# Kernel tuning notes

Measured on AMD Instinct MI355X. Metric: run time of the kernel, lower is better.

## Reference

```python
import jax, jax.numpy as jnp
import numpy as np

N_NODES = 50000
N_EDGES = 800000
N_GRAPHS = 128
IN_DIM = 256
OUT_DIM = 128
N_LAYERS = 3
NEG_SLOPE = 0.01  # nn.LeakyReLU default


def setup_inputs() -> dict:
    key = jax.random.key(0)
    ks = jax.random.split(key, 10)
    feat = jax.random.normal(ks[0], (N_NODES, IN_DIM), jnp.float32)
    src = jax.random.randint(ks[1], (N_EDGES,), 0, N_NODES, jnp.int32)
    dst = jax.random.randint(ks[2], (N_EDGES,), 0, N_NODES, jnp.int32)
    graph_ids = jnp.sort(jax.random.randint(ks[3], (N_NODES,), 0, N_GRAPHS, jnp.int32))
    s_in = 1.0 / np.sqrt(IN_DIM).astype(np.float32)
    s_out = 1.0 / np.sqrt(OUT_DIM).astype(np.float32)
    w_red = jax.random.uniform(ks[4], (IN_DIM, OUT_DIM), jnp.float32, -s_in, s_in)
    b_red = jax.random.uniform(ks[5], (OUT_DIM,), jnp.float32, -s_in, s_in)
    w_gcn = jax.random.uniform(ks[6], (N_LAYERS, OUT_DIM, OUT_DIM), jnp.float32, -s_out, s_out)
    b_gcn = jnp.zeros((N_LAYERS, OUT_DIM), jnp.float32)  # DGL GraphConv bias init = zeros
    w_cls = jax.random.uniform(ks[7], (OUT_DIM, 2), jnp.float32, -s_out, s_out)
    b_cls = jax.random.uniform(ks[8], (2,), jnp.float32, -s_out, s_out)
    return dict(feat=feat, src=src, dst=dst, graph_ids=graph_ids,
                w_red=w_red, b_red=b_red, w_gcn=w_gcn, b_gcn=b_gcn,
                w_cls=w_cls, b_cls=b_cls)


def _graph_conv(x, src, dst, w, b, out_norm, in_norm):
    # DGL GraphConv, norm='both': h = D_in^{-1/2} A D_out^{-1/2} x W + b
    xs = x * out_norm[:, None]                                   # [N, d] source normalization
    agg = jax.ops.segment_sum(xs[src], dst, num_segments=x.shape[0])  # gather -> scatter-add
    return (agg * in_norm[:, None]) @ w + b


def reference(feat, src, dst, graph_ids, w_red, b_red, w_gcn, b_gcn, w_cls, b_cls):
    n = feat.shape[0]
    ones = jnp.ones((src.shape[0],), feat.dtype)
    out_deg = jax.ops.segment_sum(ones, src, num_segments=n)
    in_deg = jax.ops.segment_sum(ones, dst, num_segments=n)
    out_norm = jnp.maximum(out_deg, 1.0) ** -0.5  # DGL clamps degree to >=1
    in_norm = jnp.maximum(in_deg, 1.0) ** -0.5
    h0 = feat @ w_red + b_red  # Dropout(0.2) in eval mode = identity
    # Faithful to source: every layer consumes h0 (node_features never updated);
    # only the last layer's activation survives the loop.
    out = h0
    for i in range(N_LAYERS):
        out = jax.nn.leaky_relu(
            _graph_conv(h0, src, dst, w_gcn[i], b_gcn[i], out_norm, in_norm), NEG_SLOPE)
    g = jax.ops.segment_sum(out, graph_ids, num_segments=N_GRAPHS)  # sum readout per graph
    return g @ w_cls + b_cls  # [N_GRAPHS, 2]
```

## Files before the change

kernel.cpp:

```cpp
#include <hip/hip_runtime.h>

#define N_NODES 50000
#define N_EDGES 800000
#define N_GRAPHS 128
#define IN_DIM 256
#define OUT_DIM 128
#define NEG_SLOPE 0.01f

#define RCHUNK 64
#define NB_SCAN ((N_NODES + 255) / 256)

#define NSLICE 4
#define SLICE 12544
#define NTOT (NSLICE * SLICE)
#define NCHUNK 64
#define NE4 (N_EDGES / 4)
#define QPC (NE4 / NCHUNK)

typedef __attribute__((ext_vector_type(8))) short bf16x8;
typedef __attribute__((ext_vector_type(4))) float f32x4;
typedef unsigned short ushort_t;
typedef unsigned int uint_t;

__device__ inline ushort_t f2b(float f) {
    union { float f; unsigned u; } c{f};
    unsigned r = c.u + 0x7FFFu + ((c.u >> 16) & 1u);
    return (ushort_t)(r >> 16);
}
__device__ inline float b2f(ushort_t u) {
    union { unsigned u; float f; } c{(unsigned)u << 16};
    return c.f;
}
__device__ inline float blo(uint_t v) {
    union { unsigned u; float f; } c{v << 16};
    return c.f;
}
__device__ inline float bhi(uint_t v) {
    union { unsigned u; float f; } c{v & 0xFFFF0000u};
    return c.f;
}

__global__ __launch_bounds__(256) void deg_kernel(const int4* __restrict__ src4,
                                                  const int4* __restrict__ dst4,
                                                  ushort_t* __restrict__ rep) {
    __shared__ int bins[SLICE];
    int b     = blockIdx.x;
    int hist  = b >> 8;
    int rem   = b & 255;
    int slice = rem >> 6;
    int chunk = rem & 63;
    const int4* ea = hist ? dst4 : src4;
    int lo = slice * SLICE;

    for (int i = threadIdx.x; i < SLICE; i += 256) bins[i] = 0;
    __syncthreads();

    int q0 = chunk * QPC;
    int q1 = q0 + QPC;
    for (int q = q0 + threadIdx.x; q < q1; q += 256) {
        int4 e = ea[q];
        unsigned a0 = (unsigned)(e.x - lo); if (a0 < SLICE) atomicAdd(&bins[a0], 1);
        unsigned a1 = (unsigned)(e.y - lo); if (a1 < SLICE) atomicAdd(&bins[a1], 1);
        unsigned a2 = (unsigned)(e.z - lo); if (a2 < SLICE) atomicAdd(&bins[a2], 1);
        unsigned a3 = (unsigned)(e.w - lo); if (a3 < SLICE) atomicAdd(&bins[a3], 1);
    }
    __syncthreads();

    uint_t* rp32 = (uint_t*)(rep + (size_t)(hist * NCHUNK + chunk) * NTOT + lo);
    for (int i = threadIdx.x; i < SLICE / 2; i += 256)
        rp32[i] = (uint_t)(bins[2 * i] | (bins[2 * i + 1] << 16));
}

__global__ __launch_bounds__(256) void norm_kernel(ushort_t* __restrict__ rep,
                                                   float* __restrict__ out_norm,
                                                   float* __restrict__ in_norm,
                                                   int* __restrict__ deg_in_tot,
                                                   int* __restrict__ bsum) {
    __shared__ int red[256];
    int t = threadIdx.x;
    int i = blockIdx.x * 256 + t;
    int si_keep = 0;
    if (i < N_NODES) {
        int so = 0;
#pragma unroll
        for (int c = 0; c < NCHUNK; ++c) so += rep[(size_t)c * NTOT + i];
        int si = 0;
#pragma unroll
        for (int c = 0; c < NCHUNK; ++c) {
            size_t off = (size_t)(NCHUNK + c) * NTOT + i;
            int v = rep[off];
            rep[off] = (ushort_t)si;
            si += v;
        }
        deg_in_tot[i] = si;
        si_keep = si;
        int dq = so > 1 ? so : 1;
        int di = si > 1 ? si : 1;
        out_norm[i] = rsqrtf((float)dq);
        in_norm[i]  = rsqrtf((float)di);
    }
    red[t] = si_keep;
    __syncthreads();
    for (int off = 128; off > 0; off >>= 1) {
        if (t < off) red[t] += red[t + off];
        __syncthreads();
    }
    if (t == 0) bsum[blockIdx.x] = red[0];
}

__global__ __launch_bounds__(256) void fill_kernel(const int* __restrict__ deg_in,
                                                   const int* __restrict__ bsum,
                                                   int* __restrict__ row_ofs) {
    __shared__ int sh[256];
    int t   = threadIdx.x;
    int bid = blockIdx.x;

    int v = (t < NB_SCAN) ? bsum[t] : 0;
    sh[t] = v;
    __syncthreads();
    for (int off = 1; off < 256; off <<= 1) {
        int a = sh[t];
        int b = (t >= off) ? sh[t - off] : 0;
        __syncthreads();
        sh[t] = a + b;
        __syncthreads();
    }
    int bofs  = sh[bid] - bsum[bid];
    int total = sh[NB_SCAN - 1];
    __syncthreads();

    int idx = bid * 256 + t;
    int dv  = (idx < N_NODES) ? deg_in[idx] : 0;
    sh[t] = dv;
    __syncthreads();
    for (int off = 1; off < 256; off <<= 1) {
        int a = sh[t];
        int b = (t >= off) ? sh[t - off] : 0;
        __syncthreads();
        sh[t] = a + b;
        __syncthreads();
    }
    if (idx < N_NODES) row_ofs[idx] = bofs + sh[t] - dv;
    if (bid == 0 && t == 0) row_ofs[N_NODES] = total;
}

__global__ __launch_bounds__(256) void build_kernel(const int4* __restrict__ src4,
                                                    const int4* __restrict__ dst4,
                                                    const int* __restrict__ row_ofs,
                                                    const ushort_t* __restrict__ rep,
                                                    int* __restrict__ esrc) {
    __shared__ int cur[SLICE];
    int b     = blockIdx.x;
    int slice = b >> 6;
    int chunk = b & 63;
    int lo    = slice * SLICE;
    const ushort_t* rel = rep + (size_t)(NCHUNK + chunk) * NTOT + lo;

    for (int i = threadIdx.x; i < SLICE; i += 256) {
        int n = lo + i;
        int r = (n < N_NODES) ? row_ofs[n] : 0;
        cur[i] = r + (int)rel[i];
    }
    __syncthreads();

    int q0 = chunk * QPC;
    int q1 = q0 + QPC;
    for (int q = q0 + threadIdx.x; q < q1; q += 256) {
        int4 s = src4[q];
        int4 d = dst4[q];
        unsigned a0 = (unsigned)(d.x - lo); if (a0 < SLICE) esrc[atomicAdd(&cur[a0], 1)] = s.x;
        unsigned a1 = (unsigned)(d.y - lo); if (a1 < SLICE) esrc[atomicAdd(&cur[a1], 1)] = s.y;
        unsigned a2 = (unsigned)(d.z - lo); if (a2 < SLICE) esrc[atomicAdd(&cur[a2], 1)] = s.z;
        unsigned a3 = (unsigned)(d.w - lo); if (a3 < SLICE) esrc[atomicAdd(&cur[a3], 1)] = s.w;
    }
}

__global__ __launch_bounds__(128) void wc_kernel(const float* __restrict__ w_red,
                                                 const float* __restrict__ b_red,
                                                 const float* __restrict__ w2,
                                                 ushort_t* __restrict__ Wcs,
                                                 float* __restrict__ bc,
                                                 float* __restrict__ g) {
    int j = threadIdx.x;
    int i = blockIdx.x;
    if (i < N_GRAPHS) g[i * OUT_DIM + j] = 0.f;
    const float* vin = (i < IN_DIM) ? (w_red + (size_t)i * OUT_DIM) : b_red;
    float s = 0.f;
    for (int k = 0; k < OUT_DIM; ++k) s = fmaf(vin[k], w2[k * OUT_DIM + j], s);
    if (i < IN_DIM) Wcs[(size_t)j * IN_DIM + i] = f2b(s);
    else            bc[j] = s;
}

__global__ __launch_bounds__(256) void gemm_z(const float* __restrict__ feat,
                                              const ushort_t* __restrict__ Wcs,
                                              const float* __restrict__ bc,
                                              const float* __restrict__ out_norm,
                                              ushort_t* __restrict__ zb) {
    __shared__ ushort_t Bs[64 * IN_DIM];
    int t    = threadIdx.x;
    int lane = t & 63;
    int wv   = t >> 6;
    int bm   = blockIdx.x * 64 + wv * 16;
    int bn0  = blockIdx.y * 64;
    int mrow = lane & 15;
    int kg   = lane >> 4;
    int gm   = bm + mrow;

    {
        const char* wsrc = (const char*)(Wcs + (size_t)bn0 * IN_DIM);
        char* bdst = (char*)Bs;
#pragma unroll
        for (int p = 0; p < 8; ++p) {
            int d  = p * 4096 + t * 16;
            int ds = d ^ (((d >> 9) & 7) << 4);
            *(int4*)(bdst + ds) = *(const int4*)(wsrc + d);
        }
    }
    __syncthreads();

    f32x4 acc[4];
#pragma unroll
    for (int nt = 0; nt < 4; ++nt) acc[nt] = (f32x4){0.f, 0.f, 0.f, 0.f};

    int boff[4];
#pragma unroll
    for (int nt = 0; nt < 4; ++nt) {
        int n = nt * 16 + mrow;
        boff[nt] = n * 512 + ((kg * 16) ^ ((n & 7) << 4));
    }
    const char* bsp = (const char*)Bs;

    bool valid = gm < N_NODES;
    const float* fp = feat + (size_t)(valid ? gm : 0) * IN_DIM + kg * 8;
    const float4 zf4 = make_float4(0.f, 0.f, 0.f, 0.f);

    float4 a0c = valid ? *(const float4*)(fp + 0) : zf4;
    float4 a1c = valid ? *(const float4*)(fp + 4) : zf4;
    float4 a0n = zf4, a1n = zf4;

#pragma unroll
    for (int kt = 0; kt < IN_DIM / 32; ++kt) {
        if (kt < IN_DIM / 32 - 1) {
            a0n = valid ? *(const float4*)(fp + (kt + 1) * 32) : zf4;
            a1n = valid ? *(const float4*)(fp + (kt + 1) * 32 + 4) : zf4;
        }
        bf16x8 af;
        af[0] = (short)f2b(a0c.x); af[1] = (short)f2b(a0c.y);
        af[2] = (short)f2b(a0c.z); af[3] = (short)f2b(a0c.w);
        af[4] = (short)f2b(a1c.x); af[5] = (short)f2b(a1c.y);
        af[6] = (short)f2b(a1c.z); af[7] = (short)f2b(a1c.w);
#pragma unroll
        for (int nt = 0; nt < 4; ++nt) {
            bf16x8 bf = *(const bf16x8*)(bsp + (boff[nt] ^ (kt << 6)));
            acc[nt] = __builtin_amdgcn_mfma_f32_16x16x32_bf16(af, bf, acc[nt], 0, 0, 0);
        }
        a0c = a0n; a1c = a1n;
    }

    float on[4];
#pragma unroll
    for (int r = 0; r < 4; ++r) {
        int row = bm + kg * 4 + r;
        on[r] = (row < N_NODES) ? out_norm[row] : 0.f;
    }
#pragma unroll
    for (int nt = 0; nt < 4; ++nt) {
        int col = bn0 + nt * 16 + mrow;
        float bcv = bc[col];
#pragma unroll
        for (int r = 0; r < 4; ++r) {
            int row = bm + kg * 4 + r;
            if (row < N_NODES)
                zb[(size_t)row * OUT_DIM + col] = f2b(on[r] * (acc[nt][r] + bcv));
        }
    }
}

__global__ __launch_bounds__(256) void gather_kernel(const uint4* __restrict__ zb4,
                                                     const int* __restrict__ esrc,
                                                     const int* __restrict__ row_ofs,
                                                     const float* __restrict__ in_norm,
                                                     const float* __restrict__ b2,
                                                     uint4* __restrict__ hb4) {
    int n      = blockIdx.x * 16 + (threadIdx.x >> 4);
    int lane16 = threadIdx.x & 15;
    int e0 = row_ofs[n];
    int e1 = row_ofs[n + 1];
    float ac[8];
#pragma unroll
    for (int i = 0; i < 8; ++i) ac[i] = 0.f;

    int e = e0;
    for (; e + 8 <= e1; e += 8) {
        uint4 v[8];
#pragma unroll
        for (int u = 0; u < 8; ++u) v[u] = zb4[(size_t)esrc[e + u] * 16 + lane16];
#pragma unroll
        for (int u = 0; u < 8; ++u) {
            ac[0] += blo(v[u].x); ac[1] += bhi(v[u].x);
            ac[2] += blo(v[u].y); ac[3] += bhi(v[u].y);
            ac[4] += blo(v[u].z); ac[5] += bhi(v[u].z);
            ac[6] += blo(v[u].w); ac[7] += bhi(v[u].w);
        }
    }
    if (e + 4 <= e1) {
        uint4 v[4];
#pragma unroll
        for (int u = 0; u < 4; ++u) v[u] = zb4[(size_t)esrc[e + u] * 16 + lane16];
#pragma unroll
        for (int u = 0; u < 4; ++u) {
            ac[0] += blo(v[u].x); ac[1] += bhi(v[u].x);
            ac[2] += blo(v[u].y); ac[3] += bhi(v[u].y);
            ac[4] += blo(v[u].z); ac[5] += bhi(v[u].z);
            ac[6] += blo(v[u].w); ac[7] += bhi(v[u].w);
        }
        e += 4;
    }
    for (; e < e1; ++e) {
        uint4 v = zb4[(size_t)esrc[e] * 16 + lane16];
        ac[0] += blo(v.x); ac[1] += bhi(v.x);
        ac[2] += blo(v.y); ac[3] += bhi(v.y);
        ac[4] += blo(v.z); ac[5] += bhi(v.z);
        ac[6] += blo(v.w); ac[7] += bhi(v.w);
    }

    float inn = in_norm[n];
    float4 bA = *(const float4*)&b2[lane16 * 8];
    float4 bB = *(const float4*)&b2[lane16 * 8 + 4];
    float hv[8];
    hv[0] = fmaf(inn, ac[0], bA.x); hv[1] = fmaf(inn, ac[1], bA.y);
    hv[2] = fmaf(inn, ac[2], bA.z); hv[3] = fmaf(inn, ac[3], bA.w);
    hv[4] = fmaf(inn, ac[4], bB.x); hv[5] = fmaf(inn, ac[5], bB.y);
    hv[6] = fmaf(inn, ac[6], bB.z); hv[7] = fmaf(inn, ac[7], bB.w);
#pragma unroll
    for (int i = 0; i < 8; ++i) hv[i] = (hv[i] > 0.f) ? hv[i] : NEG_SLOPE * hv[i];
    uint4 o;
    o.x = (uint_t)f2b(hv[0]) | ((uint_t)f2b(hv[1]) << 16);
    o.y = (uint_t)f2b(hv[2]) | ((uint_t)f2b(hv[3]) << 16);
    o.z = (uint_t)f2b(hv[4]) | ((uint_t)f2b(hv[5]) << 16);
    o.w = (uint_t)f2b(hv[6]) | ((uint_t)f2b(hv[7]) << 16);
    hb4[(size_t)n * 16 + lane16] = o;
}

__global__ __launch_bounds__(64) void readout_kernel(const uint_t* __restrict__ hb2,
                                                     const int* __restrict__ gids,
                                                     float* __restrict__ g) {
    int t    = threadIdx.x;
    int n0   = blockIdx.x * RCHUNK;
    int nend = n0 + RCHUNK;
    if (nend > N_NODES) nend = N_NODES;
    float acc0 = 0.f, acc1 = 0.f;
    int   cur = gids[n0];
    for (int n = n0; n < nend; ++n) {
        int gid = gids[n];
        if (gid != cur) {
            atomicAdd(&g[cur * OUT_DIM + 2 * t], acc0);
            atomicAdd(&g[cur * OUT_DIM + 2 * t + 1], acc1);
            acc0 = acc1 = 0.f;
            cur = gid;
        }
        uint_t v = hb2[(size_t)n * 64 + t];
        acc0 += blo(v);
        acc1 += bhi(v);
    }
    atomicAdd(&g[cur * OUT_DIM + 2 * t], acc0);
    atomicAdd(&g[cur * OUT_DIM + 2 * t + 1], acc1);
}

__global__ __launch_bounds__(256) void cls_kernel(const float* __restrict__ g,
                                                  const float* __restrict__ w_cls,
                                                  const float* __restrict__ b_cls,
                                                  float* __restrict__ out) {
    int t  = threadIdx.x;
    int gr = t >> 1;
    int c  = t & 1;
    float s = b_cls[c];
    for (int k = 0; k < OUT_DIM; ++k) s = fmaf(g[gr * OUT_DIM + k], w_cls[k * 2 + c], s);
    out[t] = s;
}

extern "C" void kernel_launch(void* const* d_in, const int* in_sizes, int n_in,
                              void* d_out, int out_size, void* d_ws, size_t ws_size,
                              hipStream_t stream) {
    const float* feat  = (const float*)d_in[0];
    const int*   src   = (const int*)d_in[1];
    const int*   dst   = (const int*)d_in[2];
    const int*   gids  = (const int*)d_in[3];
    const float* w_red = (const float*)d_in[4];
    const float* b_red = (const float*)d_in[5];
    const float* w_gcn = (const float*)d_in[6];
    const float* b_gcn = (const float*)d_in[7];
    const float* w_cls = (const float*)d_in[8];
    const float* b_cls = (const float*)d_in[9];
    float* out = (float*)d_out;

    float* z        = (float*)d_ws;
    float* h        = z + (size_t)N_NODES * OUT_DIM;
    float* out_norm = h + (size_t)N_NODES * OUT_DIM;
    float* in_norm  = out_norm + N_NODES;
    int*   deg_in   = (int*)(in_norm + N_NODES);
    int*   row_ofs  = deg_in + N_NODES;
    int*   esrc     = row_ofs + N_NODES + 1;
    int*   bsum     = esrc + N_EDGES;
    ushort_t* Wcs   = (ushort_t*)(bsum + NB_SCAN);
    float* bc       = (float*)(Wcs + IN_DIM * OUT_DIM);
    float* g        = bc + OUT_DIM;

    ushort_t* zb = (ushort_t*)z;
    ushort_t* hb = (ushort_t*)h;

    ushort_t* rep = (ushort_t*)z;

    const float* w2 = w_gcn + 2 * OUT_DIM * OUT_DIM;
    const float* b2 = b_gcn + 2 * OUT_DIM;

    deg_kernel<<<2 * NSLICE * NCHUNK, 256, 0, stream>>>((const int4*)src, (const int4*)dst, rep);
    norm_kernel<<<NB_SCAN, 256, 0, stream>>>(rep, out_norm, in_norm, deg_in, bsum);
    fill_kernel<<<NB_SCAN, 256, 0, stream>>>(deg_in, bsum, row_ofs);
    build_kernel<<<NSLICE * NCHUNK, 256, 0, stream>>>((const int4*)src, (const int4*)dst,
                                                      row_ofs, rep, esrc);
    wc_kernel<<<IN_DIM + 1, OUT_DIM, 0, stream>>>(w_red, b_red, w2, Wcs, bc, g);
    gemm_z<<<dim3((N_NODES + 63) / 64, 2), 256, 0, stream>>>(feat, Wcs, bc, out_norm, zb);
    gather_kernel<<<N_NODES / 16, 256, 0, stream>>>((const uint4*)zb, esrc, row_ofs,
                                                    in_norm, b2, (uint4*)hb);
    readout_kernel<<<(N_NODES + RCHUNK - 1) / RCHUNK, 64, 0, stream>>>((const uint_t*)hb,
                                                                       gids, g);
    cls_kernel<<<1, 256, 0, stream>>>(g, w_cls, b_cls, out);
}
```

Before: 155.5 us.

## Pack degree bins, fuse scan with weight-combine kernel, narrow gemm N tile

The degree histogram now packs two 16-bit counters per 32-bit LDS word, halving shared memory and letting the packed word be written out directly. The row-offset scan and the combined-weight precompute are merged into one launch, removing a kernel boundary. The feature GEMM now uses a 32-column tile with four column blocks instead of 64 columns with two, reducing LDS per block and raising block count. In exchange, each feature row is read from global memory four times instead of twice.

New measurement: 162.4 us. 1.04x slower.

```diff
diff --git a/kernel.cpp b/kernel.cpp
--- a/kernel.cpp
+++ b/kernel.cpp
@@ -43,7 +43,7 @@
 __global__ __launch_bounds__(256) void deg_kernel(const int4* __restrict__ src4,
                                                   const int4* __restrict__ dst4,
                                                   ushort_t* __restrict__ rep) {
-    __shared__ int bins[SLICE];
+    __shared__ uint_t bins[SLICE / 2];
     int b     = blockIdx.x;
     int hist  = b >> 8;
     int rem   = b & 255;
@@ -52,23 +52,27 @@
     const int4* ea = hist ? dst4 : src4;
     int lo = slice * SLICE;
 
-    for (int i = threadIdx.x; i < SLICE; i += 256) bins[i] = 0;
+    for (int i = threadIdx.x; i < SLICE / 2; i += 256) bins[i] = 0;
     __syncthreads();
 
     int q0 = chunk * QPC;
     int q1 = q0 + QPC;
     for (int q = q0 + threadIdx.x; q < q1; q += 256) {
         int4 e = ea[q];
-        unsigned a0 = (unsigned)(e.x - lo); if (a0 < SLICE) atomicAdd(&bins[a0], 1);
-        unsigned a1 = (unsigned)(e.y - lo); if (a1 < SLICE) atomicAdd(&bins[a1], 1);
-        unsigned a2 = (unsigned)(e.z - lo); if (a2 < SLICE) atomicAdd(&bins[a2], 1);
-        unsigned a3 = (unsigned)(e.w - lo); if (a3 < SLICE) atomicAdd(&bins[a3], 1);
+        unsigned a0 = (unsigned)(e.x - lo);
+        if (a0 < SLICE) atomicAdd(&bins[a0 >> 1], 1u << ((a0 & 1) << 4));
+        unsigned a1 = (unsigned)(e.y - lo);
+        if (a1 < SLICE) atomicAdd(&bins[a1 >> 1], 1u << ((a1 & 1) << 4));
+        unsigned a2 = (unsigned)(e.z - lo);
+        if (a2 < SLICE) atomicAdd(&bins[a2 >> 1], 1u << ((a2 & 1) << 4));
+        unsigned a3 = (unsigned)(e.w - lo);
+        if (a3 < SLICE) atomicAdd(&bins[a3 >> 1], 1u << ((a3 & 1) << 4));
     }
     __syncthreads();
 
     uint_t* rp32 = (uint_t*)(rep + (size_t)(hist * NCHUNK + chunk) * NTOT + lo);
     for (int i = threadIdx.x; i < SLICE / 2; i += 256)
-        rp32[i] = (uint_t)(bins[2 * i] | (bins[2 * i + 1] << 16));
+        rp32[i] = bins[i];
 }
 
 __global__ __launch_bounds__(256) void norm_kernel(ushort_t* __restrict__ rep,
@@ -108,40 +112,57 @@
     if (t == 0) bsum[blockIdx.x] = red[0];
 }
 
-__global__ __launch_bounds__(256) void fill_kernel(const int* __restrict__ deg_in,
-                                                   const int* __restrict__ bsum,
-                                                   int* __restrict__ row_ofs) {
-    __shared__ int sh[256];
+__global__ __launch_bounds__(256) void fillwc_kernel(const int* __restrict__ deg_in,
+                                                     const int* __restrict__ bsum,
+                                                     int* __restrict__ row_ofs,
+                                                     const float* __restrict__ w_red,
+                                                     const float* __restrict__ b_red,
+                                                     const float* __restrict__ w2,
+                                                     ushort_t* __restrict__ Wcs,
+                                                     float* __restrict__ bc,
+                                                     float* __restrict__ g) {
     int t   = threadIdx.x;
     int bid = blockIdx.x;
 
-    int v = (t < NB_SCAN) ? bsum[t] : 0;
-    sh[t] = v;
-    __syncthreads();
-    for (int off = 1; off < 256; off <<= 1) {
-        int a = sh[t];
-        int b = (t >= off) ? sh[t - off] : 0;
+    if (bid < NB_SCAN) {
+        __shared__ int sh[256];
+        int v = (t < NB_SCAN) ? bsum[t] : 0;
+        sh[t] = v;
         __syncthreads();
-        sh[t] = a + b;
+        for (int off = 1; off < 256; off <<= 1) {
+            int a = sh[t];
+            int b = (t >= off) ? sh[t - off] : 0;
+            __syncthreads();
+            sh[t] = a + b;
+            __syncthreads();
+        }
+        int bofs  = sh[bid] - bsum[bid];
+        int total = sh[NB_SCAN - 1];
         __syncthreads();
-    }
-    int bofs  = sh[bid] - bsum[bid];
-    int total = sh[NB_SCAN - 1];
-    __syncthreads();
-
-    int idx = bid * 256 + t;
-    int dv  = (idx < N_NODES) ? deg_in[idx] : 0;
-    sh[t] = dv;
-    __syncthreads();
-    for (int off = 1; off < 256; off <<= 1) {
-        int a = sh[t];
-        int b = (t >= off) ? sh[t - off] : 0;
+
+        int idx = bid * 256 + t;
+        int dv  = (idx < N_NODES) ? deg_in[idx] : 0;
+        sh[t] = dv;
         __syncthreads();
-        sh[t] = a + b;
-        __syncthreads();
-    }
-    if (idx < N_NODES) row_ofs[idx] = bofs + sh[t] - dv;
-    if (bid == 0 && t == 0) row_ofs[N_NODES] = total;
+        for (int off = 1; off < 256; off <<= 1) {
+            int a = sh[t];
+            int b = (t >= off) ? sh[t - off] : 0;
+            __syncthreads();
+            sh[t] = a + b;
+            __syncthreads();
+        }
+        if (idx < N_NODES) row_ofs[idx] = bofs + sh[t] - dv;
+        if (bid == 0 && t == 0) row_ofs[N_NODES] = total;
+    } else if (t < OUT_DIM) {
+        int i = bid - NB_SCAN;
+        int j = t;
+        if (i < N_GRAPHS) g[i * OUT_DIM + j] = 0.f;
+        const float* vin = (i < IN_DIM) ? (w_red + (size_t)i * OUT_DIM) : b_red;
+        float s = 0.f;
+        for (int k = 0; k < OUT_DIM; ++k) s = fmaf(vin[k], w2[k * OUT_DIM + j], s);
+        if (i < IN_DIM) Wcs[(size_t)j * IN_DIM + i] = f2b(s);
+        else            bc[j] = s;
+    }
 }
 
 __global__ __launch_bounds__(256) void build_kernel(const int4* __restrict__ src4,
@@ -175,33 +196,17 @@
     }
 }
 
-__global__ __launch_bounds__(128) void wc_kernel(const float* __restrict__ w_red,
-                                                 const float* __restrict__ b_red,
-                                                 const float* __restrict__ w2,
-                                                 ushort_t* __restrict__ Wcs,
-                                                 float* __restrict__ bc,
-                                                 float* __restrict__ g) {
-    int j = threadIdx.x;
-    int i = blockIdx.x;
-    if (i < N_GRAPHS) g[i * OUT_DIM + j] = 0.f;
-    const float* vin = (i < IN_DIM) ? (w_red + (size_t)i * OUT_DIM) : b_red;
-    float s = 0.f;
-    for (int k = 0; k < OUT_DIM; ++k) s = fmaf(vin[k], w2[k * OUT_DIM + j], s);
-    if (i < IN_DIM) Wcs[(size_t)j * IN_DIM + i] = f2b(s);
-    else            bc[j] = s;
-}
-
 __global__ __launch_bounds__(256) void gemm_z(const float* __restrict__ feat,
                                               const ushort_t* __restrict__ Wcs,
                                               const float* __restrict__ bc,
                                               const float* __restrict__ out_norm,
                                               ushort_t* __restrict__ zb) {
-    __shared__ ushort_t Bs[64 * IN_DIM];
+    __shared__ ushort_t Bs[32 * IN_DIM];
     int t    = threadIdx.x;
     int lane = t & 63;
     int wv   = t >> 6;
     int bm   = blockIdx.x * 64 + wv * 16;
-    int bn0  = blockIdx.y * 64;
+    int bn0  = blockIdx.y * 32;
     int mrow = lane & 15;
     int kg   = lane >> 4;
     int gm   = bm + mrow;
@@ -210,7 +215,7 @@
         const char* wsrc = (const char*)(Wcs + (size_t)bn0 * IN_DIM);
         char* bdst = (char*)Bs;
 #pragma unroll
-        for (int p = 0; p < 8; ++p) {
+        for (int p = 0; p < 4; ++p) {
             int d  = p * 4096 + t * 16;
             int ds = d ^ (((d >> 9) & 7) << 4);
             *(int4*)(bdst + ds) = *(const int4*)(wsrc + d);
@@ -218,13 +223,13 @@
     }
     __syncthreads();
 
-    f32x4 acc[4];
-#pragma unroll
-    for (int nt = 0; nt < 4; ++nt) acc[nt] = (f32x4){0.f, 0.f, 0.f, 0.f};
-
-    int boff[4];
-#pragma unroll
-    for (int nt = 0; nt < 4; ++nt) {
+    f32x4 acc[2];
+#pragma unroll
+    for (int nt = 0; nt < 2; ++nt) acc[nt] = (f32x4){0.f, 0.f, 0.f, 0.f};
+
+    int boff[2];
+#pragma unroll
+    for (int nt = 0; nt < 2; ++nt) {
         int n = nt * 16 + mrow;
         boff[nt] = n * 512 + ((kg * 16) ^ ((n & 7) << 4));
     }
@@ -250,7 +255,7 @@
         af[4] = (short)f2b(a1c.x); af[5] = (short)f2b(a1c.y);
         af[6] = (short)f2b(a1c.z); af[7] = (short)f2b(a1c.w);
 #pragma unroll
-        for (int nt = 0; nt < 4; ++nt) {
+        for (int nt = 0; nt < 2; ++nt) {
             bf16x8 bf = *(const bf16x8*)(bsp + (boff[nt] ^ (kt << 6)));
             acc[nt] = __builtin_amdgcn_mfma_f32_16x16x32_bf16(af, bf, acc[nt], 0, 0, 0);
         }
@@ -264,7 +269,7 @@
         on[r] = (row < N_NODES) ? out_norm[row] : 0.f;
     }
 #pragma unroll
-    for (int nt = 0; nt < 4; ++nt) {
+    for (int nt = 0; nt < 2; ++nt) {
         int col = bn0 + nt * 16 + mrow;
         float bcv = bc[col];
 #pragma unroll
@@ -416,11 +421,11 @@
 
     deg_kernel<<<2 * NSLICE * NCHUNK, 256, 0, stream>>>((const int4*)src, (const int4*)dst, rep);
     norm_kernel<<<NB_SCAN, 256, 0, stream>>>(rep, out_norm, in_norm, deg_in, bsum);
-    fill_kernel<<<NB_SCAN, 256, 0, stream>>>(deg_in, bsum, row_ofs);
+    fillwc_kernel<<<NB_SCAN + IN_DIM + 1, 256, 0, stream>>>(deg_in, bsum, row_ofs,
+                                                            w_red, b_red, w2, Wcs, bc, g);
     build_kernel<<<NSLICE * NCHUNK, 256, 0, stream>>>((const int4*)src, (const int4*)dst,
                                                       row_ofs, rep, esrc);
-    wc_kernel<<<IN_DIM + 1, OUT_DIM, 0, stream>>>(w_red, b_red, w2, Wcs, bc, g);
-    gemm_z<<<dim3((N_NODES + 63) / 64, 2), 256, 0, stream>>>(feat, Wcs, bc, out_norm, zb);
+    gemm_z<<<dim3((N_NODES + 63) / 64, 4), 256, 0, stream>>>(feat, Wcs, bc, out_norm, zb);
     gather_kernel<<<N_NODES / 16, 256, 0, stream>>>((const uint4*)zb, esrc, row_ofs,
                                                     in_norm, b2, (uint4*)hb);
     readout_kernel<<<(N_NODES + RCHUNK - 1) / RCHUNK, 64, 0, stream>>>((const uint_t*)hb,
```
